# Kernel tuning notes

Measured on AMD Instinct MI355X. Metric: run time of the kernel, lower is better.

The kernel has to match this reference:

```python
import jax, jax.numpy as jnp
import numpy as np
from jax import lax

K = 3      # reassembly kernel size
UP = 2     # upsample factor


def setup_inputs() -> dict:
    key = jax.random.key(0)
    ks = jax.random.split(key, 4)
    N, C, H, W = 4, 256, 128, 128
    outC = 256
    x = jax.random.normal(ks[0], (N, C, H, W), dtype=jnp.float32)
    w_down = jax.random.normal(ks[1], (C // 4, C), dtype=jnp.float32) * 0.05
    b_down = jnp.zeros((C // 4,), dtype=jnp.float32)
    w_enc = jax.random.normal(ks[2], (UP * UP * K * K, C // 4, K, K), dtype=jnp.float32) * 0.05
    b_enc = jnp.zeros((UP * UP * K * K,), dtype=jnp.float32)
    w_out = jax.random.normal(ks[3], (outC, C), dtype=jnp.float32) * 0.05
    b_out = jnp.zeros((outC,), dtype=jnp.float32)
    return {"x": x, "w_down": w_down, "b_down": b_down,
            "w_enc": w_enc, "b_enc": b_enc, "w_out": w_out, "b_out": b_out}


def _carafe_upsample(x, w_down, b_down, w_enc, b_enc, w_out, b_out):
    N, C, H, W = x.shape
    k2, up2 = K * K, UP * UP
    # kernel prediction branch: 1x1 down conv, 3x3 encoder conv
    t = jnp.einsum('oc,nchw->nohw', w_down, x) + b_down[None, :, None, None]
    enc = lax.conv_general_dilated(
        t, w_enc, window_strides=(1, 1), padding=((K // 2, K // 2), (K // 2, K // 2)),
        dimension_numbers=('NCHW', 'OIHW', 'NCHW')) + b_enc[None, :, None, None]
    # torch encoder channel layout is kk*up2 + ij; pixel_shuffle + softmax(dim=1)
    # + unfold(up,up) is equivalent to softmax over the k^2 axis here.
    enc = enc.reshape(N, k2, up2, H, W)
    kernel = jax.nn.softmax(enc, axis=1)                 # [N,k2,up2,H,W]
    kernel = kernel.transpose(0, 3, 4, 1, 2)             # [N,H,W,k2,up2]
    # extract kxk patches (zero pad), ordering di*K+dj matches torch unfold
    pad = K // 2
    xp = jnp.pad(x, ((0, 0), (0, 0), (pad, pad), (pad, pad)))
    patches = jnp.stack([xp[:, :, di:di + H, dj:dj + W]
                         for di in range(K) for dj in range(K)], axis=-1)  # [N,C,H,W,k2]
    # per-pixel reassembly matmul
    out = jnp.einsum('nchwk,nhwkq->nchwq', patches, kernel)  # [N,C,H,W,up2]
    # pixel_shuffle: channel index c*up2 + i*UP + j -> (h*UP+i, w*UP+j)
    out = out.reshape(N, C, H, W, UP, UP).transpose(0, 1, 2, 4, 3, 5)
    out = out.reshape(N, C, H * UP, W * UP)
    # final 1x1 conv
    return jnp.einsum('oc,nchw->nohw', w_out, out) + b_out[None, :, None, None]


def reference(x, w_down, b_down, w_enc, b_enc, w_out, b_out):
    return _carafe_upsample(x, w_down, b_down, w_enc, b_enc, w_out, b_out)
```

## Files before the change

kernel.cpp:

```cpp
#include <hip/hip_runtime.h>
#include <hip/hip_bf16.h>
#include <stddef.h>

typedef __attribute__((ext_vector_type(8))) short short8;
typedef __attribute__((ext_vector_type(4))) short short4v;
typedef __attribute__((ext_vector_type(4))) unsigned short ushort4v;
typedef __attribute__((ext_vector_type(4))) float floatx4;

#define N_ 4
#define C_ 256
#define H_ 128
#define W_ 128
#define HW_ (H_*W_)
#define NPX_ (N_*HW_)
#define E_ 36
#define OC_ 256

static __device__ __forceinline__ unsigned short f2bf(float f) {
    union { float f; unsigned u; } v; v.f = f;
    unsigned r = v.u + 0x7fff + ((v.u >> 16) & 1);
    return (unsigned short)(r >> 16);
}
static __device__ __forceinline__ float bf2f(unsigned short s) {
    union { unsigned u; float f; } v; v.u = ((unsigned)s) << 16;
    return v.f;
}

__global__ __launch_bounds__(256) void k_prep(const float* __restrict__ wo,
                                              const float* __restrict__ wd,
                                              short* __restrict__ wcomb,
                                              const float* __restrict__ we,
                                              unsigned short* __restrict__ wBT) {
    int bx = blockIdx.x;
    if (bx < 80) {
        int i = (bx * 256 + threadIdx.x) * 4;
        int row = i >> 8, c = i & 255;
        const float* src = (row < 256) ? &wo[row * 256 + c] : &wd[(row - 256) * 256 + c];
        float4 v = *(const float4*)src;
        short4v s;
        s.x = (short)f2bf(v.x); s.y = (short)f2bf(v.y);
        s.z = (short)f2bf(v.z); s.w = (short)f2bf(v.w);
        *(short4v*)&wcomb[i] = s;
    } else {
        int idx = (bx - 80) * 256 + threadIdx.x;
        if (idx < 48 * 576) {
            int e = idx / 576;
            int k = idx - e * 576;
            int tap = k >> 6, c = k & 63;
            float v = (e < E_) ? we[((size_t)e * 64 + c) * 9 + tap] : 0.f;
            wBT[idx] = f2bf(v);
        }
    }
}

__global__ __launch_bounds__(512, 4) void k_gemm(
    const float* __restrict__ x, const short* __restrict__ wcomb,
    const float* __restrict__ bd,
    unsigned short* __restrict__ Gq, unsigned short* __restrict__ t)
{
    __shared__ short Bsm[2][64 * 40];

    int tid = threadIdx.x;
    int bx = blockIdx.x;
    int n = bx >> 8;
    int px0 = (bx & 255) * 64;

    int lane = tid & 63;
    int wave = tid >> 6;
    int wm = wave >> 1, wn = wave & 1;

    int bpx = tid & 63, bcq = tid >> 6;
    const float* xb = x + (size_t)n * C_ * HW_ + px0 + bpx;

    int aoff[5];
    #pragma unroll
    for (int fm = 0; fm < 5; fm++) {
        int row = wm * 80 + fm * 16 + (lane & 15);
        aoff[fm] = row * 256 + ((lane >> 4) << 3);
    }

    float xs[2][4];
    short8 aw[5], an[5];

    auto xload = [&](int c0, int slot) {
        #pragma unroll
        for (int j = 0; j < 4; j++)
            xs[slot][j] = xb[(size_t)(c0 + bcq * 4 + j) * HW_];
    };
    auto commit = [&](int buf, int slot) {
        short4v bv;
        bv.x = (short)f2bf(xs[slot][0]);
        bv.y = (short)f2bf(xs[slot][1]);
        bv.z = (short)f2bf(xs[slot][2]);
        bv.w = (short)f2bf(xs[slot][3]);
        *(short4v*)&Bsm[buf][bpx * 40 + bcq * 4] = bv;
    };

    floatx4 acc[5][2];
    #pragma unroll
    for (int fm = 0; fm < 5; fm++) {
        acc[fm][0] = (floatx4)0.f;
        acc[fm][1] = (floatx4)0.f;
    }

    xload(0, 0);
    #pragma unroll
    for (int fm = 0; fm < 5; fm++)
        aw[fm] = *(const short8*)&wcomb[aoff[fm]];
    commit(0, 0);
    xload(32, 1);
    __syncthreads();

    #pragma unroll
    for (int kc = 0; kc < 8; kc++) {
        int cur = kc & 1;
        if (kc < 6) xload((kc + 2) * 32, kc & 1);
        if (kc < 7) {
            #pragma unroll
            for (int fm = 0; fm < 5; fm++)
                an[fm] = *(const short8*)&wcomb[aoff[fm] + (kc + 1) * 32];
        }
        #pragma unroll
        for (int fn = 0; fn < 2; fn++) {
            int col = wn * 32 + fn * 16 + (lane & 15);
            short8 bf = *(const short8*)&Bsm[cur][col * 40 + (lane >> 4) * 8];
            #pragma unroll
            for (int fm = 0; fm < 5; fm++)
                acc[fm][fn] = __builtin_amdgcn_mfma_f32_16x16x32_bf16(aw[fm], bf, acc[fm][fn], 0, 0, 0);
        }
        if (kc < 7) {
            commit(cur ^ 1, (kc + 1) & 1);
            #pragma unroll
            for (int fm = 0; fm < 5; fm++) aw[fm] = an[fm];
            __syncthreads();
        }
    }

    #pragma unroll
    for (int fm = 0; fm < 5; fm++) {
        int row0 = wm * 80 + fm * 16;
        if (row0 < 256) {
            int oq = (row0 >> 2) + (lane >> 4);
            #pragma unroll
            for (int fn = 0; fn < 2; fn++) {
                int col = px0 + wn * 32 + fn * 16 + (lane & 15);
                ushort4v v;
                v.x = f2bf(acc[fm][fn][0]);
                v.y = f2bf(acc[fm][fn][1]);
                v.z = f2bf(acc[fm][fn][2]);
                v.w = f2bf(acc[fm][fn][3]);
                *(ushort4v*)&Gq[(((size_t)n * 64 + oq) * HW_ + col) * 4] = v;
            }
        } else {
            int ot = row0 - 256 + ((lane >> 4) << 2);
            float b0 = bd[ot + 0], b1 = bd[ot + 1], b2 = bd[ot + 2], b3 = bd[ot + 3];
            #pragma unroll
            for (int fn = 0; fn < 2; fn++) {
                int col = px0 + wn * 32 + fn * 16 + (lane & 15);
                ushort4v r;
                r.x = f2bf(acc[fm][fn][0] + b0);
                r.y = f2bf(acc[fm][fn][1] + b1);
                r.z = f2bf(acc[fm][fn][2] + b2);
                r.w = f2bf(acc[fm][fn][3] + b3);
                *(ushort4v*)&t[((size_t)n * HW_ + col) * 64 + ot] = r;
            }
        }
    }
}

__global__ __launch_bounds__(256) void k_enc(
    const unsigned short* __restrict__ t, const unsigned short* __restrict__ wBT,
    const float* __restrict__ be, unsigned short* __restrict__ kernb)
{
    __shared__ short Tl[390 * 64];
    float* El = (float*)Tl;

    int bx = blockIdx.x;
    int n = bx >> 7, h = bx & 127;
    int tid = threadIdx.x;
    int lane = tid & 63, wave = tid >> 6;

    short8 bpre[3][3];
    const unsigned short* wB0 = wBT + (size_t)(lane & 15) * 576 + (lane >> 4) * 8;
    #pragma unroll
    for (int p = 0; p < 2; p++)
        #pragma unroll
        for (int fn = 0; fn < 3; fn++)
            bpre[p][fn] = *(const short8*)(wB0 + fn * 16 * 576 + p * 32);

    for (int idx = tid; idx < 3120; idx += 256) {
        int r = idx >> 3, ch = idx & 7;
        int di = r / 130, rr = r - di * 130;
        int hh = h + di - 1, ww = rr - 1;
        short8 v = {0,0,0,0,0,0,0,0};
        if (hh >= 0 && hh < H_ && ww >= 0 && ww < W_)
            v = *(const short8*)&t[((size_t)(n * H_ + hh) * W_ + ww) * 64 + ch * 8];
        int us = (r * 64 + ch * 8) ^ ((r & 7) << 3);
        *(short8*)&Tl[us] = v;
    }
    __syncthreads();

    floatx4 acc[2][3];
    #pragma unroll
    for (int mf = 0; mf < 2; mf++)
        #pragma unroll
        for (int fn = 0; fn < 3; fn++)
            acc[mf][fn] = (floatx4)0.f;

    int pxw = wave * 32 + (lane & 15);
    int kq = (lane >> 4) * 8;

    #pragma unroll
    for (int kc = 0; kc < 18; kc++) {
        if (kc < 16) {
            int slot = (kc + 2) % 3;
            #pragma unroll
            for (int fn = 0; fn < 3; fn++)
                bpre[slot][fn] = *(const short8*)(wB0 + fn * 16 * 576 + (kc + 2) * 32);
        }
        const int cur = kc % 3;
        const int tap = kc >> 1, chalf = kc & 1;
        const int di = tap / 3, dj = tap % 3;
        #pragma unroll
        for (int mf = 0; mf < 2; mf++) {
            int r = di * 130 + pxw + mf * 16 + dj;
            int us = (r * 64 + chalf * 32 + kq) ^ ((r & 7) << 3);
            short8 af = *(const short8*)&Tl[us];
            #pragma unroll
            for (int fn = 0; fn < 3; fn++)
                acc[mf][fn] = __builtin_amdgcn_mfma_f32_16x16x32_bf16(af, bpre[cur][fn], acc[mf][fn], 0, 0, 0);
        }
    }
    __syncthreads();

    #pragma unroll
    for (int mf = 0; mf < 2; mf++)
        #pragma unroll
        for (int fn = 0; fn < 3; fn++)
            #pragma unroll
            for (int i = 0; i < 4; i++) {
                int px = wave * 32 + mf * 16 + (lane >> 4) * 4 + i;
                El[px * 49 + fn * 16 + (lane & 15)] = acc[mf][fn][i];
            }
    __syncthreads();

    int sp = tid >> 1;
    int pxg = n * HW_ + h * W_ + sp;
    #pragma unroll
    for (int qq = 0; qq < 2; qq++) {
        int q = (tid & 1) * 2 + qq;
        float l[9];
        #pragma unroll
        for (int k = 0; k < 9; k++) l[k] = El[sp * 49 + k * 4 + q] + be[k * 4 + q];
        float m = l[0];
        #pragma unroll
        for (int k = 1; k < 9; k++) m = fmaxf(m, l[k]);
        float ex[9], s = 0.f;
        #pragma unroll
        for (int k = 0; k < 9; k++) { ex[k] = __expf(l[k] - m); s += ex[k]; }
        float inv = 1.f / s;
        #pragma unroll
        for (int k = 0; k < 9; k++)
            kernb[(size_t)(k * 4 + q) * NPX_ + pxg] = f2bf(ex[k] * inv);
    }
}

__global__ __launch_bounds__(256) void k_up(
    const unsigned short* __restrict__ Gq, const unsigned short* __restrict__ kernb,
    const float* __restrict__ bo, float* __restrict__ y)
{
    int bx = blockIdx.x;
    int x7 = bx & 7;
    int g  = bx >> 3;
    int hbhi = g & 7;
    int og = (g >> 3) & 7;
    int n  = g >> 6;
    int hb = hbhi * 8 + x7;

    int tid = threadIdx.x;
    int h = hb * 2 + (tid >> 7);
    int w = tid & 127;
    int idxp = n * HW_ + h * W_ + w;

    float kv[36];
    #pragma unroll
    for (int e = 0; e < E_; e++)
        kv[e] = bf2f(kernb[(size_t)e * NPX_ + idxp]);

    int off[9]; bool val[9];
    #pragma unroll
    for (int di = 0; di < 3; di++) {
        int hh = h + di - 1;
        bool hvv = (hh >= 0 && hh < H_);
        int hc = hvv ? hh : h;
        #pragma unroll
        for (int dj = 0; dj < 3; dj++) {
            int ww = w + dj - 1;
            bool wvv = (ww >= 0 && ww < W_);
            int wc = wvv ? ww : w;
            off[di * 3 + dj] = hc * W_ + wc;
            val[di * 3 + dj] = hvv && wvv;
        }
    }

    const unsigned short* Gb = Gq + ((size_t)n * 64 + og * 8) * HW_ * 4;
    size_t ybase = ((size_t)n * OC_ + og * 32) * (4 * HW_) + (size_t)(2 * h) * 256 + 2 * w;

    #pragma unroll 2
    for (int j = 0; j < 8; j++) {
        const unsigned short* Gj = Gb + (size_t)j * HW_ * 4;
        float b0 = bo[og * 32 + j * 4 + 0];
        float b1 = bo[og * 32 + j * 4 + 1];
        float b2 = bo[og * 32 + j * 4 + 2];
        float b3 = bo[og * 32 + j * 4 + 3];
        float a[4][4];
        #pragma unroll
        for (int s = 0; s < 4; s++) { a[0][s] = b0; a[1][s] = b1; a[2][s] = b2; a[3][s] = b3; }
        #pragma unroll
        for (int k = 0; k < 9; k++) {
            ushort4v gv = *(const ushort4v*)(Gj + (size_t)off[k] * 4);
            float g0 = val[k] ? bf2f(gv.x) : 0.f;
            float g1 = val[k] ? bf2f(gv.y) : 0.f;
            float g2 = val[k] ? bf2f(gv.z) : 0.f;
            float g3 = val[k] ? bf2f(gv.w) : 0.f;
            #pragma unroll
            for (int s = 0; s < 4; s++) {
                float kw = kv[k * 4 + s];
                a[0][s] = fmaf(g0, kw, a[0][s]);
                a[1][s] = fmaf(g1, kw, a[1][s]);
                a[2][s] = fmaf(g2, kw, a[2][s]);
                a[3][s] = fmaf(g3, kw, a[3][s]);
            }
        }
        #pragma unroll
        for (int i = 0; i < 4; i++) {
            float* yp = y + ybase + (size_t)(j * 4 + i) * (4 * HW_);
            float2 r0; r0.x = a[i][0]; r0.y = a[i][1];
            float2 r1; r1.x = a[i][2]; r1.y = a[i][3];
            *(float2*)yp = r0;
            *(float2*)(yp + 256) = r1;
        }
    }
}

extern "C" void kernel_launch(void* const* d_in, const int* in_sizes, int n_in,
                              void* d_out, int out_size, void* d_ws, size_t ws_size,
                              hipStream_t stream) {
    const float* x  = (const float*)d_in[0];
    const float* wd = (const float*)d_in[1];
    const float* bd = (const float*)d_in[2];
    const float* we = (const float*)d_in[3];
    const float* be = (const float*)d_in[4];
    const float* wo = (const float*)d_in[5];
    const float* bo = (const float*)d_in[6];
    float* y = (float*)d_out;

    unsigned short* t = (unsigned short*)d_ws;
    unsigned short* kernb = t + (size_t)NPX_ * 64;
    short* wcomb = (short*)(kernb + (size_t)E_ * NPX_);
    unsigned short* wBT = (unsigned short*)(wcomb + (size_t)320 * C_);
    unsigned short* Gq  = wBT + (size_t)48 * 576;

    k_prep<<<188,  256, 0, stream>>>(wo, wd, wcomb, we, wBT);
    k_gemm<<<1024, 512, 0, stream>>>(x, wcomb, bd, Gq, t);
    k_enc <<<512,  256, 0, stream>>>(t, wBT, be, kernb);
    k_up  <<<2048, 256, 0, stream>>>(Gq, kernb, bo, y);
}
```

Measured before the change: 136.4 us.

## Pad Gq with zero halo and store softmax kernel weights pixel-major

The intermediate Gq tensor is now stored in a 130x130 padded layout whose border is zeroed in the prep kernel, so the upsample kernel reads 3x3 neighbours without bounds checks or masking. The softmax kernel weights are now written per pixel as 36 contiguous bf16 values, so each thread loads them with nine vector loads instead of 36 strided scalar loads. The cost is a larger Gq buffer, extra prep work to zero the halo, and half the k_enc threads sitting idle during the softmax step.

```diff
diff --git a/kernel.cpp b/kernel.cpp
--- a/kernel.cpp
+++ b/kernel.cpp
@@ -15,6 +15,8 @@
 #define NPX_ (N_*HW_)
 #define E_ 36
 #define OC_ 256
+#define GP_ 130
+#define GSZ_ (GP_*GP_)
 
 static __device__ __forceinline__ unsigned short f2bf(float f) {
     union { float f; unsigned u; } v; v.f = f;
@@ -30,7 +32,8 @@
                                               const float* __restrict__ wd,
                                               short* __restrict__ wcomb,
                                               const float* __restrict__ we,
-                                              unsigned short* __restrict__ wBT) {
+                                              unsigned short* __restrict__ wBT,
+                                              unsigned short* __restrict__ Gq) {
     int bx = blockIdx.x;
     if (bx < 80) {
         int i = (bx * 256 + threadIdx.x) * 4;
@@ -41,7 +44,7 @@
         s.x = (short)f2bf(v.x); s.y = (short)f2bf(v.y);
         s.z = (short)f2bf(v.z); s.w = (short)f2bf(v.w);
         *(short4v*)&wcomb[i] = s;
-    } else {
+    } else if (bx < 188) {
         int idx = (bx - 80) * 256 + threadIdx.x;
         if (idx < 48 * 576) {
             int e = idx / 576;
@@ -49,6 +52,19 @@
             int tap = k >> 6, c = k & 63;
             float v = (e < E_) ? we[((size_t)e * 64 + c) * 9 + tap] : 0.f;
             wBT[idx] = f2bf(v);
+        }
+    } else {
+        unsigned idx = (bx - 188) * 256 + threadIdx.x;
+        if (idx < 256u * 516u) {
+            unsigned combo = idx / 516u;
+            unsigned c = idx - combo * 516u;
+            unsigned pos;
+            if (c < 130u)      pos = c;
+            else if (c < 260u) pos = 129u * GP_ + (c - 130u);
+            else if (c < 388u) pos = (c - 260u + 1u) * GP_;
+            else               pos = (c - 388u + 1u) * GP_ + 129u;
+            ushort4v z = {0, 0, 0, 0};
+            *(ushort4v*)&Gq[((size_t)combo * GSZ_ + pos) * 4] = z;
         }
     }
 }
@@ -144,12 +160,14 @@
             #pragma unroll
             for (int fn = 0; fn < 2; fn++) {
                 int col = px0 + wn * 32 + fn * 16 + (lane & 15);
+                int hh = col >> 7, ww = col & 127;
                 ushort4v v;
                 v.x = f2bf(acc[fm][fn][0]);
                 v.y = f2bf(acc[fm][fn][1]);
                 v.z = f2bf(acc[fm][fn][2]);
                 v.w = f2bf(acc[fm][fn][3]);
-                *(ushort4v*)&Gq[(((size_t)n * 64 + oq) * HW_ + col) * 4] = v;
+                size_t cell = ((size_t)n * 64 + oq) * GSZ_ + (hh + 1) * GP_ + ww + 1;
+                *(ushort4v*)&Gq[cell * 4] = v;
             }
         } else {
             int ot = row0 - 256 + ((lane >> 4) << 2);
@@ -244,24 +262,32 @@
             }
     __syncthreads();
 
-    int sp = tid >> 1;
-    int pxg = n * HW_ + h * W_ + sp;
-    #pragma unroll
-    for (int qq = 0; qq < 2; qq++) {
-        int q = (tid & 1) * 2 + qq;
-        float l[9];
-        #pragma unroll
-        for (int k = 0; k < 9; k++) l[k] = El[sp * 49 + k * 4 + q] + be[k * 4 + q];
-        float m = l[0];
-        #pragma unroll
-        for (int k = 1; k < 9; k++) m = fmaxf(m, l[k]);
-        float ex[9], s = 0.f;
-        #pragma unroll
-        for (int k = 0; k < 9; k++) { ex[k] = __expf(l[k] - m); s += ex[k]; }
-        float inv = 1.f / s;
-        #pragma unroll
-        for (int k = 0; k < 9; k++)
-            kernb[(size_t)(k * 4 + q) * NPX_ + pxg] = f2bf(ex[k] * inv);
+    if (tid < 128) {
+        int sp = tid;
+        unsigned short out[36];
+        #pragma unroll
+        for (int q = 0; q < 4; q++) {
+            float l[9];
+            #pragma unroll
+            for (int k = 0; k < 9; k++) l[k] = El[sp * 49 + k * 4 + q] + be[k * 4 + q];
+            float m = l[0];
+            #pragma unroll
+            for (int k = 1; k < 9; k++) m = fmaxf(m, l[k]);
+            float ex[9], s = 0.f;
+            #pragma unroll
+            for (int k = 0; k < 9; k++) { ex[k] = __expf(l[k] - m); s += ex[k]; }
+            float inv = 1.f / s;
+            #pragma unroll
+            for (int k = 0; k < 9; k++) out[k * 4 + q] = f2bf(ex[k] * inv);
+        }
+        unsigned short* kp = kernb + (size_t)(n * HW_ + h * W_ + sp) * 36;
+        #pragma unroll
+        for (int i = 0; i < 9; i++) {
+            ushort4v v4;
+            v4.x = out[i * 4]; v4.y = out[i * 4 + 1];
+            v4.z = out[i * 4 + 2]; v4.w = out[i * 4 + 3];
+            *(ushort4v*)&kp[i * 4] = v4;
+        }
     }
 }
 
@@ -283,32 +309,24 @@
     int idxp = n * HW_ + h * W_ + w;
 
     float kv[36];
-    #pragma unroll
-    for (int e = 0; e < E_; e++)
-        kv[e] = bf2f(kernb[(size_t)e * NPX_ + idxp]);
-
-    int off[9]; bool val[9];
-    #pragma unroll
-    for (int di = 0; di < 3; di++) {
-        int hh = h + di - 1;
-        bool hvv = (hh >= 0 && hh < H_);
-        int hc = hvv ? hh : h;
-        #pragma unroll
-        for (int dj = 0; dj < 3; dj++) {
-            int ww = w + dj - 1;
-            bool wvv = (ww >= 0 && ww < W_);
-            int wc = wvv ? ww : w;
-            off[di * 3 + dj] = hc * W_ + wc;
-            val[di * 3 + dj] = hvv && wvv;
-        }
-    }
-
-    const unsigned short* Gb = Gq + ((size_t)n * 64 + og * 8) * HW_ * 4;
+    {
+        const unsigned short* kp = kernb + (size_t)idxp * 36;
+        #pragma unroll
+        for (int i = 0; i < 9; i++) {
+            ushort4v v4 = *(const ushort4v*)&kp[i * 4];
+            kv[i * 4 + 0] = bf2f(v4.x);
+            kv[i * 4 + 1] = bf2f(v4.y);
+            kv[i * 4 + 2] = bf2f(v4.z);
+            kv[i * 4 + 3] = bf2f(v4.w);
+        }
+    }
+
+    const size_t gcenter = (size_t)(h + 1) * GP_ + (w + 1);
     size_t ybase = ((size_t)n * OC_ + og * 32) * (4 * HW_) + (size_t)(2 * h) * 256 + 2 * w;
 
     #pragma unroll 2
     for (int j = 0; j < 8; j++) {
-        const unsigned short* Gj = Gb + (size_t)j * HW_ * 4;
+        const unsigned short* Gj = Gq + (((size_t)n * 64 + og * 8 + j) * GSZ_ + gcenter) * 4;
         float b0 = bo[og * 32 + j * 4 + 0];
         float b1 = bo[og * 32 + j * 4 + 1];
         float b2 = bo[og * 32 + j * 4 + 2];
@@ -317,21 +335,21 @@
         #pragma unroll
         for (int s = 0; s < 4; s++) { a[0][s] = b0; a[1][s] = b1; a[2][s] = b2; a[3][s] = b3; }
         #pragma unroll
-        for (int k = 0; k < 9; k++) {
-            ushort4v gv = *(const ushort4v*)(Gj + (size_t)off[k] * 4);
-            float g0 = val[k] ? bf2f(gv.x) : 0.f;
-            float g1 = val[k] ? bf2f(gv.y) : 0.f;
-            float g2 = val[k] ? bf2f(gv.z) : 0.f;
-            float g3 = val[k] ? bf2f(gv.w) : 0.f;
-            #pragma unroll
-            for (int s = 0; s < 4; s++) {
-                float kw = kv[k * 4 + s];
-                a[0][s] = fmaf(g0, kw, a[0][s]);
-                a[1][s] = fmaf(g1, kw, a[1][s]);
-                a[2][s] = fmaf(g2, kw, a[2][s]);
-                a[3][s] = fmaf(g3, kw, a[3][s]);
+        for (int di = 0; di < 3; di++)
+            #pragma unroll
+            for (int dj = 0; dj < 3; dj++) {
+                int k = di * 3 + dj;
+                ushort4v gv = *(const ushort4v*)(Gj + ((di - 1) * GP_ + (dj - 1)) * 4);
+                float g0 = bf2f(gv.x), g1 = bf2f(gv.y), g2 = bf2f(gv.z), g3 = bf2f(gv.w);
+                #pragma unroll
+                for (int s = 0; s < 4; s++) {
+                    float kw = kv[k * 4 + s];
+                    a[0][s] = fmaf(g0, kw, a[0][s]);
+                    a[1][s] = fmaf(g1, kw, a[1][s]);
+                    a[2][s] = fmaf(g2, kw, a[2][s]);
+                    a[3][s] = fmaf(g3, kw, a[3][s]);
+                }
             }
-        }
         #pragma unroll
         for (int i = 0; i < 4; i++) {
             float* yp = y + ybase + (size_t)(j * 4 + i) * (4 * HW_);
@@ -357,11 +375,11 @@
 
     unsigned short* t = (unsigned short*)d_ws;
     unsigned short* kernb = t + (size_t)NPX_ * 64;
-    short* wcomb = (short*)(kernb + (size_t)E_ * NPX_);
+    short* wcomb = (short*)(kernb + (size_t)NPX_ * E_);
     unsigned short* wBT = (unsigned short*)(wcomb + (size_t)320 * C_);
     unsigned short* Gq  = wBT + (size_t)48 * 576;
 
-    k_prep<<<188,  256, 0, stream>>>(wo, wd, wcomb, we, wBT);
+    k_prep<<<704,  256, 0, stream>>>(wo, wd, wcomb, we, wBT, Gq);
     k_gemm<<<1024, 512, 0, stream>>>(x, wcomb, bd, Gq, t);
     k_enc <<<512,  256, 0, stream>>>(t, wBT, be, kernb);
     k_up  <<<2048, 256, 0, stream>>>(Gq, kernb, bo, y);
```

Measured after the change: 143.3 us. 1.05x slower.
